# Kernel optimization log

Measured on AMD Instinct MI355X. Metric: run time of the kernel, lower is better.

The kernel has to match this reference:

```python
import jax, jax.numpy as jnp
import numpy as np

EPS = 1e-16  # torch.clamp(squared_distance, min=1e-16)


def knn_interpolate(x, pos_x, pos_y, k):
    """Faithful jax version of Mesh_Reduced.knn_interpolate.

    x:     [Nx, C]  features at source nodes
    pos_x: [Nx, 3]  source positions
    pos_y: [Ny, 3]  query positions
    Returns [Ny, C].
    """
    # Brute-force knn (replaces torch_cluster.knn). Use the expanded form
    # ||y||^2 + ||x||^2 - 2 y.x to avoid a [Ny, Nx, 3] intermediate.
    d2 = (
        jnp.sum(pos_y * pos_y, axis=-1)[:, None]
        + jnp.sum(pos_x * pos_x, axis=-1)[None, :]
        - 2.0 * pos_y @ pos_x.T
    )  # [Ny, Nx]
    _, x_idx = jax.lax.top_k(-d2, k)  # [Ny, k] nearest source indices per query

    # Exact squared distance on the selected neighbors (matches torch numerics:
    # diff = pos_x[x_idx] - pos_y[y_idx]).
    diff = pos_x[x_idx] - pos_y[:, None, :]           # [Ny, k, 3]
    sq = jnp.sum(diff * diff, axis=-1, keepdims=True)  # [Ny, k, 1]
    w = 1.0 / jnp.clip(sq, EPS)                        # inverse-distance weights

    xg = x[x_idx]                                      # gather: [Ny, k, C]
    # scatter-sum over the k neighbors of each query == reduce over axis 1
    num = jnp.sum(xg * w, axis=1)                      # [Ny, C]
    den = jnp.sum(w, axis=1)                           # [Ny, 1]
    return (num / den).astype(jnp.float32)


def setup_inputs() -> dict:
    key = jax.random.key(0)
    k1, k2, k3 = jax.random.split(key, 3)
    N_PIVOTAL, N_MESH, C = 2048, 65536, 16
    return {
        "x": jax.random.normal(k1, (N_PIVOTAL, C), dtype=jnp.float32),
        "pos_x": jax.random.uniform(k2, (N_PIVOTAL, 3), dtype=jnp.float32),
        "pos_y": jax.random.uniform(k3, (N_MESH, 3), dtype=jnp.float32),
        "k": 3,
    }


def reference(x, pos_x, pos_y, k):
    return knn_interpolate(x, pos_x, pos_y, k)
```

## Files before the change

kernel.cpp:

```cpp
#include <hip/hip_runtime.h>
#include <stdint.h>

#define NXP   2048
#define NC    16
#define GD    8
#define NCELL (GD*GD*GD)
#define BBLK  512
#define QBLK  512
#define SEG   8
#define QPB   (QBLK / SEG)

#define WS_SPT   0
#define WS_SIDX  32768
#define WS_CST   40960

__device__ __forceinline__ int cell_of(float v) {
    int c = (int)(v * (float)GD);
    c = c > GD - 1 ? GD - 1 : c;
    return c < 0 ? 0 : c;
}

__device__ __forceinline__ uint32_t mono(float d) {
    uint32_t b = __float_as_uint(d);
    return b ^ (uint32_t)(((int32_t)b >> 31) | 0x80000000);
}
__device__ __forceinline__ float unmono(uint32_t m) {
    uint32_t b = (m & 0x80000000u) ? (m ^ 0x80000000u) : ~m;
    return __uint_as_float(b);
}

__device__ __forceinline__ void ins_fast(uint64_t k, uint64_t& b0, uint64_t& b1, uint64_t& b2) {
    const bool lt0 = k < b0, lt1 = k < b1;
    b2 = lt1 ? b1 : k;
    b1 = lt0 ? b0 : (lt1 ? k : b1);
    b0 = lt0 ? k  : b0;
}

__device__ __forceinline__ void ins_dedup(uint64_t k, uint64_t& b0, uint64_t& b1, uint64_t& b2) {
    if (k == b0 || k == b1 || k == b2) return;
    const bool lt0 = k < b0, lt1 = k < b1, lt2 = k < b2;
    b2 = lt1 ? b1 : (lt2 ? k : b2);
    b1 = lt0 ? b0 : (lt1 ? k : b1);
    b0 = lt0 ? k  : b0;
}

__device__ __forceinline__ uint64_t shfl_xor_u64(uint64_t v, int mask) {
    const int lo = __shfl_xor((int)(uint32_t)v, mask);
    const int hi = __shfl_xor((int)(uint32_t)(v >> 32), mask);
    return ((uint64_t)(uint32_t)hi << 32) | (uint32_t)lo;
}

__device__ __forceinline__ void merge_group(uint64_t& b0, uint64_t& b1, uint64_t& b2) {
    #pragma unroll
    for (int mask = 1; mask < SEG; mask <<= 1) {
        const uint64_t r0 = shfl_xor_u64(b0, mask);
        const uint64_t r1 = shfl_xor_u64(b1, mask);
        const uint64_t r2 = shfl_xor_u64(b2, mask);
        ins_dedup(r0, b0, b1, b2);
        ins_dedup(r1, b0, b1, b2);
        ins_dedup(r2, b0, b1, b2);
    }
}

__global__ __launch_bounds__(BBLK) void build_grid(
    const float* __restrict__ pos_x,
    float4* __restrict__ wspt, int* __restrict__ wsidx, int* __restrict__ wcstart)
{
    __shared__ int sA[NCELL];
    __shared__ int sB[NCELL];
    __shared__ int cur[NCELL];
    const int t = threadIdx.x;

    sA[t] = 0;
    __syncthreads();

    const float4* px4 = (const float4*)pos_x;
    const float4 v0 = px4[t*3+0], v1 = px4[t*3+1], v2 = px4[t*3+2];
    const float pxx[4] = {v0.x, v0.w, v1.z, v2.y};
    const float pyy[4] = {v0.y, v1.x, v1.w, v2.z};
    const float pzz[4] = {v0.z, v1.y, v2.x, v2.w};
    int cc[4];
    #pragma unroll
    for (int i = 0; i < 4; ++i) {
        cc[i] = (cell_of(pzz[i]) * GD + cell_of(pyy[i])) * GD + cell_of(pxx[i]);
        atomicAdd(&sA[cc[i]], 1);
    }
    __syncthreads();

    int* src = sA; int* dst = sB;
    for (int off = 1; off < NCELL; off <<= 1) {
        dst[t] = src[t] + (t >= off ? src[t - off] : 0);
        __syncthreads();
        int* tmp = src; src = dst; dst = tmp;
    }
    wcstart[t + 1] = src[t];
    if (t == 0) wcstart[0] = 0;
    cur[t] = (t == 0) ? 0 : src[t - 1];
    __syncthreads();

    #pragma unroll
    for (int i = 0; i < 4; ++i) {
        const int p = t * 4 + i;
        const int pos = atomicAdd(&cur[cc[i]], 1);
        const float sx = __fadd_rn(__fadd_rn(__fmul_rn(pxx[i], pxx[i]),
                                             __fmul_rn(pyy[i], pyy[i])),
                                   __fmul_rn(pzz[i], pzz[i]));
        wspt[pos] = make_float4(pxx[i], pyy[i], pzz[i], sx);
        wsidx[pos] = p;
    }
}

__global__ __launch_bounds__(QBLK) void knn_query(
    const float* __restrict__ x,
    const float* __restrict__ pos_x,
    const float* __restrict__ pos_y,
    const float4* __restrict__ wspt, const int* __restrict__ wsidx,
    const int* __restrict__ wcstart,
    float* __restrict__ out,
    int ny)
{
    __shared__ float4 spt[NXP];
    __shared__ int    sidx[NXP];
    __shared__ int    cstart[NCELL + 1];

    const int t = threadIdx.x;

    #pragma unroll
    for (int i = t; i < NXP; i += QBLK) spt[i] = wspt[i];
    #pragma unroll
    for (int i = t; i < NXP; i += QBLK) sidx[i] = wsidx[i];
    for (int i = t; i < NCELL + 1; i += QBLK) cstart[i] = wcstart[i];
    __syncthreads();

    const int s = t & (SEG - 1);
    const int q = blockIdx.x * QPB + (t >> 3);
    if (q >= ny) return;

    const float y0 = pos_y[q*3+0], y1 = pos_y[q*3+1], y2 = pos_y[q*3+2];
    const float sy = __fadd_rn(__fadd_rn(__fmul_rn(y0, y0), __fmul_rn(y1, y1)),
                               __fmul_rn(y2, y2));
    const int cx = cell_of(y0), cy = cell_of(y1), cz = cell_of(y2);

    uint64_t b0 = ~0ull, b1 = ~0ull, b2 = ~0ull;

#define EVAL_BODY(P, INS)                                                       \
    {                                                                           \
        const float4 pt = spt[P];                                               \
        const float dot = __fmaf_rn(y2, pt.z,                                   \
                          __fmaf_rn(y1, pt.y, __fmul_rn(y0, pt.x)));            \
        const float d = __fmaf_rn(-2.0f, dot, __fadd_rn(sy, pt.w));             \
        const uint64_t kk = ((uint64_t)mono(d) << 32) | (uint32_t)sidx[P];      \
        if (kk < b2) INS(kk, b0, b1, b2);                                       \
    }

    const int x0 = cx - 1 < 0 ? 0 : cx - 1;
    const int x1 = cx + 1 > GD - 1 ? GD - 1 : cx + 1;
    #pragma unroll
    for (int r = 0; r < 9; ++r) {
        const int uz = cz + r / 3 - 1, uy = cy + r % 3 - 1;
        int st = 0, en = 0;
        if (((unsigned)uz < (unsigned)GD) & ((unsigned)uy < (unsigned)GD)) {
            const int cb = (uz * GD + uy) * GD;
            st = cstart[cb + x0];
            en = cstart[cb + x1 + 1];
        }
        for (int p = st + s; p < en; p += SEG) EVAL_BODY(p, ins_fast)
    }
    merge_group(b0, b1, b2);

    {
        bool have3 = (b2 != ~0ull);
        float b2d = unmono((uint32_t)(b2 >> 32));
        if (!(have3 && (b2d + 1e-4f < 0.015625f))) {
            for (int r = 0; r < 25; ++r) {
                const int dzi = r / 5 - 2, dyi = r % 5 - 2;
                const int uz = cz + dzi, uy = cy + dyi;
                if (((unsigned)uz >= (unsigned)GD) | ((unsigned)uy >= (unsigned)GD))
                    continue;
                const int cb = (uz * GD + uy) * GD;
                if (dzi == -2 || dzi == 2 || dyi == -2 || dyi == 2) {
                    const int xa = cx - 2 < 0 ? 0 : cx - 2;
                    const int xb = cx + 2 > GD - 1 ? GD - 1 : cx + 2;
                    const int st = cstart[cb + xa], en = cstart[cb + xb + 1];
                    for (int p = st + s; p < en; p += SEG) EVAL_BODY(p, ins_fast)
                } else {
                    if (cx - 2 >= 0) {
                        const int st = cstart[cb + cx - 2], en = cstart[cb + cx - 1];
                        for (int p = st + s; p < en; p += SEG) EVAL_BODY(p, ins_fast)
                    }
                    if (cx + 2 <= GD - 1) {
                        const int st = cstart[cb + cx + 2], en = cstart[cb + cx + 3];
                        for (int p = st + s; p < en; p += SEG) EVAL_BODY(p, ins_fast)
                    }
                }
            }
            merge_group(b0, b1, b2);

            have3 = (b2 != ~0ull);
            b2d = unmono((uint32_t)(b2 >> 32));
            if (!(have3 && (b2d + 1e-4f < 0.0625f))) {
                for (int p = s; p < NXP; p += SEG) EVAL_BODY(p, ins_dedup)
                merge_group(b0, b1, b2);
            }
        }
    }
#undef EVAL_BODY

    const int j[3] = { (int)(uint32_t)b0, (int)(uint32_t)b1, (int)(uint32_t)b2 };
    float w[3];
    #pragma unroll
    for (int i = 0; i < 3; ++i) {
        const int jj = j[i];
        const float ax = pos_x[jj*3+0], ay = pos_x[jj*3+1], az = pos_x[jj*3+2];
        const float dx = __fsub_rn(ax, y0);
        const float dy = __fsub_rn(ay, y1);
        const float dz = __fsub_rn(az, y2);
        const float sq = __fadd_rn(__fadd_rn(__fmul_rn(dx, dx), __fmul_rn(dy, dy)),
                                   __fmul_rn(dz, dz));
        w[i] = 1.0f / fmaxf(sq, 1e-16f);
    }
    const float inv_den = 1.0f / __fadd_rn(__fadd_rn(w[0], w[1]), w[2]);

    const float2* x2 = (const float2*)x;
    float2* o2 = (float2*)out;
    const float2 a = x2[j[0]*8 + s];
    const float2 b = x2[j[1]*8 + s];
    const float2 c = x2[j[2]*8 + s];
    float2 rr;
    rr.x = (w[0]*a.x + w[1]*b.x + w[2]*c.x) * inv_den;
    rr.y = (w[0]*a.y + w[1]*b.y + w[2]*c.y) * inv_den;
    o2[q*8 + s] = rr;
}

extern "C" void kernel_launch(void* const* d_in, const int* in_sizes, int n_in,
                              void* d_out, int out_size, void* d_ws, size_t ws_size,
                              hipStream_t stream) {
    const float* x     = (const float*)d_in[0];
    const float* pos_x = (const float*)d_in[1];
    const float* pos_y = (const float*)d_in[2];

    float* out = (float*)d_out;
    const int ny = in_sizes[2] / 3;

    float4* wspt   = (float4*)((char*)d_ws + WS_SPT);
    int*    wsidx  = (int*)   ((char*)d_ws + WS_SIDX);
    int*    wcst   = (int*)   ((char*)d_ws + WS_CST);

    build_grid<<<1, BBLK, 0, stream>>>(pos_x, wspt, wsidx, wcst);

    const int grid = (ny + QPB - 1) / QPB;
    knn_query<<<grid, QBLK, 0, stream>>>(x, pos_x, pos_y, wspt, wsidx, wcst, out, ny);
}
```

Measured before the change: 33.96 us.

## Use persistent query blocks and a warp-shuffle scan in grid build

The query kernel now launches a fixed grid of 512 blocks that loop over query batches. Each block loads the shared grid table once and reuses it across batches instead of reloading it in 1024 blocks. The grid builder replaces its 9-step block-wide Hillis-Steele scan, which needed a barrier per step, with a per-thread serial scan of 8 cells plus a wavefront shuffle scan over 64 threads. The risks are less parallelism for latency hiding and load imbalance when a few batches need the expensive fallback search.

```diff
diff --git a/kernel.cpp b/kernel.cpp
--- a/kernel.cpp
+++ b/kernel.cpp
@@ -9,6 +9,7 @@
 #define QBLK  512
 #define SEG   8
 #define QPB   (QBLK / SEG)
+#define QGRID 512
 
 #define WS_SPT   0
 #define WS_SIDX  32768
@@ -67,7 +68,6 @@
     float4* __restrict__ wspt, int* __restrict__ wsidx, int* __restrict__ wcstart)
 {
     __shared__ int sA[NCELL];
-    __shared__ int sB[NCELL];
     __shared__ int cur[NCELL];
     const int t = threadIdx.x;
 
@@ -87,15 +87,27 @@
     }
     __syncthreads();
 
-    int* src = sA; int* dst = sB;
-    for (int off = 1; off < NCELL; off <<= 1) {
-        dst[t] = src[t] + (t >= off ? src[t - off] : 0);
-        __syncthreads();
-        int* tmp = src; src = dst; dst = tmp;
-    }
-    wcstart[t + 1] = src[t];
-    if (t == 0) wcstart[0] = 0;
-    cur[t] = (t == 0) ? 0 : src[t - 1];
+    if (t < 64) {
+        const int base = t * 8;
+        int v[8];
+        int run = 0;
+        #pragma unroll
+        for (int i = 0; i < 8; ++i) { run += sA[base + i]; v[i] = run; }
+        int xs = run;
+        #pragma unroll
+        for (int off = 1; off < 64; off <<= 1) {
+            const int y = __shfl_up(xs, off);
+            if (t >= off) xs += y;
+        }
+        const int excl = xs - run;
+        #pragma unroll
+        for (int i = 0; i < 8; ++i) {
+            const int inc = excl + v[i];
+            wcstart[base + i + 1] = inc;
+            cur[base + i] = inc - sA[base + i];
+        }
+        if (t == 0) wcstart[0] = 0;
+    }
     __syncthreads();
 
     #pragma unroll
@@ -133,103 +145,107 @@
     __syncthreads();
 
     const int s = t & (SEG - 1);
-    const int q = blockIdx.x * QPB + (t >> 3);
-    if (q >= ny) return;
-
-    const float y0 = pos_y[q*3+0], y1 = pos_y[q*3+1], y2 = pos_y[q*3+2];
-    const float sy = __fadd_rn(__fadd_rn(__fmul_rn(y0, y0), __fmul_rn(y1, y1)),
-                               __fmul_rn(y2, y2));
-    const int cx = cell_of(y0), cy = cell_of(y1), cz = cell_of(y2);
-
-    uint64_t b0 = ~0ull, b1 = ~0ull, b2 = ~0ull;
+    const int nbatch = (ny + QPB - 1) / QPB;
+
+    for (int batch = blockIdx.x; batch < nbatch; batch += gridDim.x) {
+        const int q = batch * QPB + (t >> 3);
+        if (q >= ny) continue;
+
+        const float y0 = pos_y[q*3+0], y1 = pos_y[q*3+1], y2 = pos_y[q*3+2];
+        const float sy = __fadd_rn(__fadd_rn(__fmul_rn(y0, y0), __fmul_rn(y1, y1)),
+                                   __fmul_rn(y2, y2));
+        const int cx = cell_of(y0), cy = cell_of(y1), cz = cell_of(y2);
+
+        uint64_t b0 = ~0ull, b1 = ~0ull, b2 = ~0ull;
 
 #define EVAL_BODY(P, INS)                                                       \
-    {                                                                           \
-        const float4 pt = spt[P];                                               \
-        const float dot = __fmaf_rn(y2, pt.z,                                   \
-                          __fmaf_rn(y1, pt.y, __fmul_rn(y0, pt.x)));            \
-        const float d = __fmaf_rn(-2.0f, dot, __fadd_rn(sy, pt.w));             \
-        const uint64_t kk = ((uint64_t)mono(d) << 32) | (uint32_t)sidx[P];      \
-        if (kk < b2) INS(kk, b0, b1, b2);                                       \
-    }
-
-    const int x0 = cx - 1 < 0 ? 0 : cx - 1;
-    const int x1 = cx + 1 > GD - 1 ? GD - 1 : cx + 1;
-    #pragma unroll
-    for (int r = 0; r < 9; ++r) {
-        const int uz = cz + r / 3 - 1, uy = cy + r % 3 - 1;
-        int st = 0, en = 0;
-        if (((unsigned)uz < (unsigned)GD) & ((unsigned)uy < (unsigned)GD)) {
-            const int cb = (uz * GD + uy) * GD;
-            st = cstart[cb + x0];
-            en = cstart[cb + x1 + 1];
-        }
-        for (int p = st + s; p < en; p += SEG) EVAL_BODY(p, ins_fast)
-    }
-    merge_group(b0, b1, b2);
-
-    {
-        bool have3 = (b2 != ~0ull);
-        float b2d = unmono((uint32_t)(b2 >> 32));
-        if (!(have3 && (b2d + 1e-4f < 0.015625f))) {
-            for (int r = 0; r < 25; ++r) {
-                const int dzi = r / 5 - 2, dyi = r % 5 - 2;
-                const int uz = cz + dzi, uy = cy + dyi;
-                if (((unsigned)uz >= (unsigned)GD) | ((unsigned)uy >= (unsigned)GD))
-                    continue;
+        {                                                                       \
+            const float4 pt = spt[P];                                           \
+            const float dot = __fmaf_rn(y2, pt.z,                               \
+                              __fmaf_rn(y1, pt.y, __fmul_rn(y0, pt.x)));        \
+            const float d = __fmaf_rn(-2.0f, dot, __fadd_rn(sy, pt.w));         \
+            const uint64_t kk = ((uint64_t)mono(d) << 32) | (uint32_t)sidx[P];  \
+            if (kk < b2) INS(kk, b0, b1, b2);                                   \
+        }
+
+        const int x0 = cx - 1 < 0 ? 0 : cx - 1;
+        const int x1 = cx + 1 > GD - 1 ? GD - 1 : cx + 1;
+        #pragma unroll
+        for (int r = 0; r < 9; ++r) {
+            const int uz = cz + r / 3 - 1, uy = cy + r % 3 - 1;
+            int st = 0, en = 0;
+            if (((unsigned)uz < (unsigned)GD) & ((unsigned)uy < (unsigned)GD)) {
                 const int cb = (uz * GD + uy) * GD;
-                if (dzi == -2 || dzi == 2 || dyi == -2 || dyi == 2) {
-                    const int xa = cx - 2 < 0 ? 0 : cx - 2;
-                    const int xb = cx + 2 > GD - 1 ? GD - 1 : cx + 2;
-                    const int st = cstart[cb + xa], en = cstart[cb + xb + 1];
-                    for (int p = st + s; p < en; p += SEG) EVAL_BODY(p, ins_fast)
-                } else {
-                    if (cx - 2 >= 0) {
-                        const int st = cstart[cb + cx - 2], en = cstart[cb + cx - 1];
+                st = cstart[cb + x0];
+                en = cstart[cb + x1 + 1];
+            }
+            for (int p = st + s; p < en; p += SEG) EVAL_BODY(p, ins_fast)
+        }
+        merge_group(b0, b1, b2);
+
+        {
+            bool have3 = (b2 != ~0ull);
+            float b2d = unmono((uint32_t)(b2 >> 32));
+            if (!(have3 && (b2d + 1e-4f < 0.015625f))) {
+                for (int r = 0; r < 25; ++r) {
+                    const int dzi = r / 5 - 2, dyi = r % 5 - 2;
+                    const int uz = cz + dzi, uy = cy + dyi;
+                    if (((unsigned)uz >= (unsigned)GD) | ((unsigned)uy >= (unsigned)GD))
+                        continue;
+                    const int cb = (uz * GD + uy) * GD;
+                    if (dzi == -2 || dzi == 2 || dyi == -2 || dyi == 2) {
+                        const int xa = cx - 2 < 0 ? 0 : cx - 2;
+                        const int xb = cx + 2 > GD - 1 ? GD - 1 : cx + 2;
+                        const int st = cstart[cb + xa], en = cstart[cb + xb + 1];
                         for (int p = st + s; p < en; p += SEG) EVAL_BODY(p, ins_fast)
-                    }
-                    if (cx + 2 <= GD - 1) {
-                        const int st = cstart[cb + cx + 2], en = cstart[cb + cx + 3];
-                        for (int p = st + s; p < en; p += SEG) EVAL_BODY(p, ins_fast)
+                    } else {
+                        if (cx - 2 >= 0) {
+                            const int st = cstart[cb + cx - 2], en = cstart[cb + cx - 1];
+                            for (int p = st + s; p < en; p += SEG) EVAL_BODY(p, ins_fast)
+                        }
+                        if (cx + 2 <= GD - 1) {
+                            const int st = cstart[cb + cx + 2], en = cstart[cb + cx + 3];
+                            for (int p = st + s; p < en; p += SEG) EVAL_BODY(p, ins_fast)
+                        }
                     }
                 }
+                merge_group(b0, b1, b2);
+
+                have3 = (b2 != ~0ull);
+                b2d = unmono((uint32_t)(b2 >> 32));
+                if (!(have3 && (b2d + 1e-4f < 0.0625f))) {
+                    for (int p = s; p < NXP; p += SEG) EVAL_BODY(p, ins_dedup)
+                    merge_group(b0, b1, b2);
+                }
             }
-            merge_group(b0, b1, b2);
-
-            have3 = (b2 != ~0ull);
-            b2d = unmono((uint32_t)(b2 >> 32));
-            if (!(have3 && (b2d + 1e-4f < 0.0625f))) {
-                for (int p = s; p < NXP; p += SEG) EVAL_BODY(p, ins_dedup)
-                merge_group(b0, b1, b2);
-            }
-        }
-    }
+        }
 #undef EVAL_BODY
 
-    const int j[3] = { (int)(uint32_t)b0, (int)(uint32_t)b1, (int)(uint32_t)b2 };
-    float w[3];
-    #pragma unroll
-    for (int i = 0; i < 3; ++i) {
-        const int jj = j[i];
-        const float ax = pos_x[jj*3+0], ay = pos_x[jj*3+1], az = pos_x[jj*3+2];
-        const float dx = __fsub_rn(ax, y0);
-        const float dy = __fsub_rn(ay, y1);
-        const float dz = __fsub_rn(az, y2);
-        const float sq = __fadd_rn(__fadd_rn(__fmul_rn(dx, dx), __fmul_rn(dy, dy)),
-                                   __fmul_rn(dz, dz));
-        w[i] = 1.0f / fmaxf(sq, 1e-16f);
-    }
-    const float inv_den = 1.0f / __fadd_rn(__fadd_rn(w[0], w[1]), w[2]);
-
-    const float2* x2 = (const float2*)x;
-    float2* o2 = (float2*)out;
-    const float2 a = x2[j[0]*8 + s];
-    const float2 b = x2[j[1]*8 + s];
-    const float2 c = x2[j[2]*8 + s];
-    float2 rr;
-    rr.x = (w[0]*a.x + w[1]*b.x + w[2]*c.x) * inv_den;
-    rr.y = (w[0]*a.y + w[1]*b.y + w[2]*c.y) * inv_den;
-    o2[q*8 + s] = rr;
+        const int j[3] = { (int)(uint32_t)b0, (int)(uint32_t)b1, (int)(uint32_t)b2 };
+        float w[3];
+        #pragma unroll
+        for (int i = 0; i < 3; ++i) {
+            const int jj = j[i];
+            const float ax = pos_x[jj*3+0], ay = pos_x[jj*3+1], az = pos_x[jj*3+2];
+            const float dx = __fsub_rn(ax, y0);
+            const float dy = __fsub_rn(ay, y1);
+            const float dz = __fsub_rn(az, y2);
+            const float sq = __fadd_rn(__fadd_rn(__fmul_rn(dx, dx), __fmul_rn(dy, dy)),
+                                       __fmul_rn(dz, dz));
+            w[i] = 1.0f / fmaxf(sq, 1e-16f);
+        }
+        const float inv_den = 1.0f / __fadd_rn(__fadd_rn(w[0], w[1]), w[2]);
+
+        const float2* x2 = (const float2*)x;
+        float2* o2 = (float2*)out;
+        const float2 a = x2[j[0]*8 + s];
+        const float2 b = x2[j[1]*8 + s];
+        const float2 c = x2[j[2]*8 + s];
+        float2 rr;
+        rr.x = (w[0]*a.x + w[1]*b.x + w[2]*c.x) * inv_den;
+        rr.y = (w[0]*a.y + w[1]*b.y + w[2]*c.y) * inv_den;
+        o2[q*8 + s] = rr;
+    }
 }
 
 extern "C" void kernel_launch(void* const* d_in, const int* in_sizes, int n_in,
@@ -248,6 +264,5 @@
 
     build_grid<<<1, BBLK, 0, stream>>>(pos_x, wspt, wsidx, wcst);
 
-    const int grid = (ny + QPB - 1) / QPB;
-    knn_query<<<grid, QBLK, 0, stream>>>(x, pos_x, pos_y, wspt, wsidx, wcst, out, ny);
-}
+    knn_query<<<QGRID, QBLK, 0, stream>>>(x, pos_x, pos_y, wspt, wsidx, wcst, out, ny);
+}
```

Result: no change. 33.93 us (-0.1%).
